# Optimization experiments

Measured on AMD Instinct MI355X. Metric: run time of the kernel, lower is better.

## Reference

```python
import jax, jax.numpy as jnp
import numpy as np

B, T, F = 2048, 96, 32
H = 1024
G_EMB = 16
LSTM_IN = F + 11 + 1 + G_EMB  # 60


def _lstm_cell(x, h, c, W_ih, W_hh, b):
    g = x @ W_ih.T + h @ W_hh.T + b
    i, f, gg, o = jnp.split(g, 4, axis=-1)  # torch gate order: i, f, g, o
    c_new = jax.nn.sigmoid(f) * c + jax.nn.sigmoid(i) * jnp.tanh(gg)
    h_new = jax.nn.sigmoid(o) * jnp.tanh(c_new)
    return h_new, c_new


def setup_inputs() -> dict:
    key = jax.random.key(0)
    ks = jax.random.split(key, 26)
    s = 1.0 / np.sqrt(H)
    inp = {
        "dec_known": jax.random.normal(ks[0], (B, T, F), jnp.float32),
        "target_y": jax.random.normal(ks[1], (B, T, 1), jnp.float32),
        "enc_h": jax.random.normal(ks[2], (2, B, H), jnp.float32),
        "enc_c": jax.random.normal(ks[3], (2, B, H), jnp.float32),
        "last_enc_consumption": jax.random.normal(ks[4], (B, 1), jnp.float32),
        "group_ids": jax.random.randint(ks[5], (B,), 0, 1000),
        "cat_province": jax.random.randint(ks[6], (B,), 0, 13),
        "cat_customer_type": jax.random.randint(ks[7], (B,), 0, 2),
        "cat_price_type": jax.random.randint(ks[8], (B,), 0, 5),
        "cat_consumption_level": jax.random.randint(ks[9], (B,), 0, 3),
        # learned parameters
        "group_emb": jax.random.normal(ks[10], (1000, G_EMB), jnp.float32),
        "emb_province": jax.random.normal(ks[11], (13, 4), jnp.float32),
        "emb_customer_type": jax.random.normal(ks[12], (2, 2), jnp.float32),
        "emb_price_type": jax.random.normal(ks[13], (5, 3), jnp.float32),
        "emb_consumption_level": jax.random.normal(ks[14], (3, 2), jnp.float32),
        "W_ih0": jax.random.normal(ks[15], (4 * H, LSTM_IN), jnp.float32) * s,
        "W_hh0": jax.random.normal(ks[16], (4 * H, H), jnp.float32) * s,
        "b0": jax.random.normal(ks[17], (4 * H,), jnp.float32) * s,
        "W_ih1": jax.random.normal(ks[18], (4 * H, H), jnp.float32) * s,
        "W_hh1": jax.random.normal(ks[19], (4 * H, H), jnp.float32) * s,
        "b1": jax.random.normal(ks[20], (4 * H,), jnp.float32) * s,
        "W_proj": jax.random.normal(ks[21], (1, H), jnp.float32) * s,
        "b_proj": jnp.zeros((1,), jnp.float32),
    }
    return inp


def reference(dec_known, target_y, enc_h, enc_c, last_enc_consumption,
              group_ids, cat_province, cat_customer_type, cat_price_type,
              cat_consumption_level, group_emb, emb_province, emb_customer_type,
              emb_price_type, emb_consumption_level, W_ih0, W_hh0, b0,
              W_ih1, W_hh1, b1, W_proj, b_proj):
    b, t, _ = dec_known.shape
    # static per-sample features (categorical + group embeddings)
    cat_emb = jnp.concatenate([
        emb_province[cat_province], emb_customer_type[cat_customer_type],
        emb_price_type[cat_price_type], emb_consumption_level[cat_consumption_level],
    ], axis=-1)  # [B, 11]
    group_vec = group_emb[group_ids]  # [B, 16]
    static = jnp.concatenate([cat_emb, group_vec], axis=-1)  # [B, 27]
    # teacher_forcing_ratio = 1.0 => prev_y is last_enc_consumption then target_y shifted
    prev_y = jnp.concatenate([last_enc_consumption[:, None, :], target_y[:, :-1, :]], axis=1)  # [B,T,1]
    x = jnp.concatenate([
        prev_y, dec_known,
        jnp.broadcast_to(static[:, None, :], (b, t, static.shape[-1])),
    ], axis=-1)  # [B, T, 60]

    def step(carry, x_t):
        h1, c1, h2, c2 = carry
        h1, c1 = _lstm_cell(x_t, h1, c1, W_ih0, W_hh0, b0)
        h2, c2 = _lstm_cell(h1, h2, c2, W_ih1, W_hh1, b1)
        return (h1, c1, h2, c2), h2

    init = (enc_h[0], enc_c[0], enc_h[1], enc_c[1])
    _, hs = jax.lax.scan(step, init, jnp.swapaxes(x, 0, 1))  # hs: [T, B, H]
    y = jnp.einsum('tbh,oh->bto', hs, W_proj) + b_proj  # [B, T, 1]
    return y
```

## Files before the change

### kernel.cpp

```cpp
#include <hip/hip_runtime.h>
#include <hip/hip_bf16.h>
#include <stdint.h>


#define BB  2048
#define TT  96
#define NG  4096
#define NT0 34
#define NT1 64

typedef __bf16 bf16;
typedef __bf16 bf16x8 __attribute__((ext_vector_type(8)));
typedef float  f32x4  __attribute__((ext_vector_type(4)));

__device__ __forceinline__ float sigm(float x) { return 1.0f / (1.0f + __expf(-x)); }
__device__ __forceinline__ float ftanh(float x) { return 2.0f / (1.0f + __expf(-2.0f * x)) - 1.0f; }

#define SB() __builtin_amdgcn_sched_barrier(0)


__global__ __launch_bounds__(256) void build_wf1(const float* __restrict__ Wih1,
                                                 const float* __restrict__ Whh1,
                                                 bf16* __restrict__ Wf) {
  int idx = blockIdx.x * 256 + threadIdx.x;
  if (idx >= 16 * NT1 * 8192) return;
  int j = idx & 7, lane = (idx >> 3) & 63, gf = (idx >> 9) & 7;
  int wg = (idx >> 12) & 1, kt = (idx >> 13) & 63, panel = idx >> 19;
  int np = panel * 256 + wg * 128 + gf * 16 + (lane & 15);
  int k  = kt * 32 + ((lane >> 4) << 3) + j;
  int n  = (np & 3) * 1024 + (np >> 2);
  float v = (k < 1024) ? Wih1[n * 1024 + k] : Whh1[n * 1024 + (k - 1024)];
  Wf[idx] = (bf16)v;
}

__global__ __launch_bounds__(256) void build_wf0(const float* __restrict__ Wih0,
                                                 const float* __restrict__ Whh0,
                                                 bf16* __restrict__ Wf) {
  int idx = blockIdx.x * 256 + threadIdx.x;
  if (idx >= 16 * NT0 * 8192) return;
  int j = idx & 7, lane = (idx >> 3) & 63, gf = (idx >> 9) & 7;
  int wg = (idx >> 12) & 1;
  int rem = idx >> 13;
  int kt = rem % NT0, panel = rem / NT0;
  int np = panel * 256 + wg * 128 + gf * 16 + (lane & 15);
  int k  = kt * 32 + ((lane >> 4) << 3) + j;
  int n  = (np & 3) * 1024 + (np >> 2);
  float v;
  if (k < 60)      v = Wih0[n * 60 + k];
  else if (k < 64) v = 0.0f;
  else             v = Whh0[n * 1024 + (k - 64)];
  Wf[idx] = (bf16)v;
}

__global__ __launch_bounds__(256) void perm_bias(const float* __restrict__ b0,
                                                 const float* __restrict__ b1,
                                                 float* __restrict__ b0p,
                                                 float* __restrict__ b1p) {
  int idx = blockIdx.x * 256 + threadIdx.x;
  if (idx >= NG) return;
  int n = (idx & 3) * 1024 + (idx >> 2);
  b0p[idx] = b0[n];
  b1p[idx] = b1[n];
}

__global__ __launch_bounds__(256) void build_xf(
    const float* __restrict__ dec, const float* __restrict__ ty, const float* __restrict__ lec,
    const int* __restrict__ gid, const int* __restrict__ cp, const int* __restrict__ cct,
    const int* __restrict__ cpt, const int* __restrict__ ccl,
    const float* __restrict__ gemb, const float* __restrict__ ep, const float* __restrict__ ect,
    const float* __restrict__ ept, const float* __restrict__ ecl,
    bf16* __restrict__ Xf) {
  int idx = blockIdx.x * 256 + threadIdx.x;
  if (idx >= BB * TT) return;
  int b = idx / TT, t = idx % TT;
  float xv[64];
  xv[0] = (t == 0) ? lec[b] : ty[b * TT + t - 1];
  const float* d = dec + (size_t)idx * 32;
  #pragma unroll
  for (int k = 0; k < 32; ++k) xv[1 + k] = d[k];
  const float* e;
  e = ep  + cp[b]  * 4;  for (int j = 0; j < 4;  ++j) xv[33 + j] = e[j];
  e = ect + cct[b] * 2;  for (int j = 0; j < 2;  ++j) xv[37 + j] = e[j];
  e = ept + cpt[b] * 3;  for (int j = 0; j < 3;  ++j) xv[39 + j] = e[j];
  e = ecl + ccl[b] * 2;  for (int j = 0; j < 2;  ++j) xv[42 + j] = e[j];
  e = gemb + gid[b] * 16; for (int j = 0; j < 16; ++j) xv[44 + j] = e[j];
  for (int j = 60; j < 64; ++j) xv[j] = 0.0f;
  bf16* slab = Xf + (size_t)t * BB * 64;
  int bt = b >> 4, bl = b & 15;
  #pragma unroll
  for (int k = 0; k < 64; ++k)
    slab[((size_t)(bt * 8 + (k >> 3)) << 7) + bl * 8 + (k & 7)] = (bf16)xv[k];
}

__global__ __launch_bounds__(256) void init_state(const float* __restrict__ enc_h,
                                                  const float* __restrict__ enc_c,
                                                  bf16* __restrict__ H1b,
                                                  bf16* __restrict__ H2b,
                                                  float* __restrict__ c1t,
                                                  float* __restrict__ c2t) {
  int idx = blockIdx.x * 256 + threadIdx.x;
  if (idx >= BB * 1024) return;
  int b = idx >> 10, h = idx & 1023;
  size_t off = ((size_t)((b >> 4) * 128 + (h >> 3)) << 7) + ((b & 15) << 3) + (h & 7);
  H1b[off] = (bf16)enc_h[idx];
  H2b[off] = (bf16)enc_h[(size_t)BB * 1024 + idx];
  c1t[(size_t)h * BB + b] = enc_c[idx];
  c2t[(size_t)h * BB + b] = enc_c[(size_t)BB * 1024 + idx];
}


template <int MODE>
__device__ __forceinline__ void body(
    int tm, int tn, int t,
    const bf16* __restrict__ P0, const bf16* __restrict__ P1,
    const bf16* __restrict__ Wf, const float* __restrict__ bperm,
    float* __restrict__ ct, bf16* __restrict__ Hout,
    const float* __restrict__ wp, const float* __restrict__ bp,
    float* __restrict__ y, bf16* hst_all)
{
  constexpr int NT = MODE ? NT1 : NT0;

  const int tid = threadIdx.x;
  const int lane = tid & 63, w = tid >> 6;
  const int lrow = lane & 15, u = lane >> 4;
  const int wb = w & 1, wg = w >> 1;

  f32x4 acc[8][4];
  #pragma unroll
  for (int gf = 0; gf < 8; ++gf)
    #pragma unroll
    for (int bf = 0; bf < 4; ++bf) acc[gf][bf] = (f32x4){0.f, 0.f, 0.f, 0.f};

  const int aoff = (u << 7) + (lrow << 3);
  const int BtB = (tm >> 4) + wb * 4;

  auto loadA = [&](bf16x8 (&af)[4], int kt) {
    #pragma unroll
    for (int bf = 0; bf < 4; ++bf) {
      const bf16* p;
      if constexpr (MODE == 0) {
        p = (kt < 2) ? P0 + ((size_t)((BtB + bf) * 8 + kt * 4) << 7) + aoff
                     : P1 + ((size_t)((BtB + bf) * 128 + (kt - 2) * 4) << 7) + aoff;
      } else {
        p = (kt < 32) ? P0 + ((size_t)((BtB + bf) * 128 + kt * 4) << 7) + aoff
                      : P1 + ((size_t)((BtB + bf) * 128 + (kt - 32) * 4) << 7) + aoff;
      }
      af[bf] = *reinterpret_cast<const bf16x8*>(p);
    }
  };

  const bf16* wfbase = Wf + (size_t)(tn >> 8) * NT * 8192 + wg * 4096 + lane * 8;
  auto loadW = [&](bf16x8 (&wf)[8], int kt) {
    const bf16* p = wfbase + (size_t)kt * 8192;
    #pragma unroll
    for (int gf = 0; gf < 8; ++gf)
      wf[gf] = *reinterpret_cast<const bf16x8*>(p + gf * 512);
  };

  bf16x8 afA[4], afB[4], wfA[8], wfB[8];

  loadA(afA, 0); loadW(wfA, 0);
  for (int kt = 0; kt < NT; kt += 2) {
    if (kt + 1 < NT) { loadA(afB, kt + 1); loadW(wfB, kt + 1); }
    SB();
    __builtin_amdgcn_s_setprio(1);
    #pragma unroll
    for (int gf = 0; gf < 8; ++gf)
      #pragma unroll
      for (int bf = 0; bf < 4; ++bf)
        acc[gf][bf] = __builtin_amdgcn_mfma_f32_16x16x32_bf16(wfA[gf], afA[bf], acc[gf][bf], 0, 0, 0);
    __builtin_amdgcn_s_setprio(0);
    if (kt + 2 < NT) { loadA(afA, kt + 2); loadW(wfA, kt + 2); }
    SB();
    __builtin_amdgcn_s_setprio(1);
    #pragma unroll
    for (int gf = 0; gf < 8; ++gf)
      #pragma unroll
      for (int bf = 0; bf < 4; ++bf)
        acc[gf][bf] = __builtin_amdgcn_mfma_f32_16x16x32_bf16(wfB[gf], afB[bf], acc[gf][bf], 0, 0, 0);
    __builtin_amdgcn_s_setprio(0);
  }

  bf16* hst = hst_all + w * 2048;
  const int hq = (tn >> 2) + wg * 32;
  const int bgb = tm + wb * 64;
  float yp[4] = {0.f, 0.f, 0.f, 0.f};

  #pragma unroll
  for (int gf = 0; gf < 8; ++gf) {
    int hg = hq + gf * 4 + u;
    f32x4 bv = *reinterpret_cast<const f32x4*>(&bperm[hg * 4]);
    float wph = 0.f;
    if constexpr (MODE == 1) wph = wp[hg];
    #pragma unroll
    for (int bf = 0; bf < 4; ++bf) {
      int bg = bgb + bf * 16 + lrow;
      float gi = acc[gf][bf][0] + bv[0];
      float gf_ = acc[gf][bf][1] + bv[1];
      float gg = acc[gf][bf][2] + bv[2];
      float go = acc[gf][bf][3] + bv[3];
      float* cp_ = ct + (size_t)hg * BB + bg;
      float c = *cp_;
      float cn = sigm(gf_) * c + sigm(gi) * ftanh(gg);
      float hn = sigm(go) * ftanh(cn);
      *cp_ = cn;
      hst[(bf * 16 + lrow) * 32 + gf * 4 + u] = (bf16)hn;
      if constexpr (MODE == 1) yp[bf] += hn * wph;
    }
  }

  asm volatile("s_waitcnt lgkmcnt(0)" ::: "memory");
  SB();

  #pragma unroll
  for (int q = 0; q < 4; ++q) {
    int chunk = q * 64 + lane;
    int row = chunk >> 2, seg = chunk & 3;
    bf16x8 v = *reinterpret_cast<const bf16x8*>(&hst[row * 32 + seg * 8]);
    size_t off = ((size_t)(((bgb >> 4) + (row >> 4)) * 128 + (hq >> 3) + seg) << 7)
               + ((row & 15) << 3);
    *reinterpret_cast<bf16x8*>(&Hout[off]) = v;
  }

  if constexpr (MODE == 1) {
    #pragma unroll
    for (int bf = 0; bf < 4; ++bf) {
      float s = yp[bf];
      s += __shfl_xor(s, 16);
      s += __shfl_xor(s, 32);
      if (lane < 16)
        atomicAdd(&y[(size_t)(bgb + bf * 16 + lane) * TT + t], s);
    }
  } else {
    if (tn == 0 && tid < 128) y[(size_t)(tm + tid) * TT + t] = bp[0];
  }
}

__global__ __launch_bounds__(256, 2) void step_kernel(
    const bf16* __restrict__ H1in, const bf16* __restrict__ H2in,
    bf16* __restrict__ H1out, bf16* __restrict__ H2out,
    const bf16* __restrict__ Xf,
    const bf16* __restrict__ Wf0, const bf16* __restrict__ Wf1,
    const float* __restrict__ b0p, const float* __restrict__ b1p,
    float* __restrict__ c1t, float* __restrict__ c2t,
    const float* __restrict__ wp, const float* __restrict__ bp,
    float* __restrict__ y, int t2, int only_l1) {
  __shared__ alignas(16) bf16 hst_all[4 * 2048];
  int bid = (int)blockIdx.x;
  if (only_l1 || bid >= 256) {
    int v = only_l1 ? bid : bid - 256;
    int t1 = t2 + 1;
    if (t1 >= TT) return;
    int x = v & 7, r = v >> 3;
    int tm = (r & 15) << 7;
    int tn = ((x << 1) + (r >> 4)) << 8;
    body<0>(tm, tn, t1, Xf + (size_t)t1 * BB * 64, H1in,
            Wf0, b0p, c1t, H1out, nullptr, bp, y, hst_all);
  } else {
    int x = bid & 7, r = bid >> 3;
    int tm = (r & 15) << 7;
    int tn = ((x << 1) + (r >> 4)) << 8;
    body<1>(tm, tn, t2, H1in, H2in,
            Wf1, b1p, c2t, H2out, wp, nullptr, y, hst_all);
  }
}


extern "C" void kernel_launch(void* const* d_in, const int* in_sizes, int n_in,
                              void* d_out, int out_size, void* d_ws, size_t ws_size,
                              hipStream_t stream) {
  const float* dec   = (const float*)d_in[0];
  const float* ty    = (const float*)d_in[1];
  const float* enc_h = (const float*)d_in[2];
  const float* enc_c = (const float*)d_in[3];
  const float* lec   = (const float*)d_in[4];
  const int*   gid   = (const int*)d_in[5];
  const int*   cp    = (const int*)d_in[6];
  const int*   cct   = (const int*)d_in[7];
  const int*   cpt   = (const int*)d_in[8];
  const int*   ccl   = (const int*)d_in[9];
  const float* gemb  = (const float*)d_in[10];
  const float* ep    = (const float*)d_in[11];
  const float* ect   = (const float*)d_in[12];
  const float* ept   = (const float*)d_in[13];
  const float* ecl   = (const float*)d_in[14];
  const float* Wih0  = (const float*)d_in[15];
  const float* Whh0  = (const float*)d_in[16];
  const float* b0    = (const float*)d_in[17];
  const float* Wih1  = (const float*)d_in[18];
  const float* Whh1  = (const float*)d_in[19];
  const float* b1    = (const float*)d_in[20];
  const float* wp    = (const float*)d_in[21];
  const float* bp    = (const float*)d_in[22];
  float* y = (float*)d_out;

  char* ws = (char*)d_ws;
  bf16* Wf1   = (bf16*)ws;  ws += (size_t)16 * NT1 * 8192 * 2;
  bf16* Wf0   = (bf16*)ws;  ws += (size_t)16 * NT0 * 8192 * 2;
  bf16* Xf    = (bf16*)ws;  ws += (size_t)BB * TT * 64 * 2;
  bf16* H1a   = (bf16*)ws;  ws += (size_t)BB * 1024 * 2;
  bf16* H1b   = (bf16*)ws;  ws += (size_t)BB * 1024 * 2;
  bf16* H2a   = (bf16*)ws;  ws += (size_t)BB * 1024 * 2;
  bf16* H2b   = (bf16*)ws;  ws += (size_t)BB * 1024 * 2;
  float* c1t  = (float*)ws; ws += (size_t)BB * 1024 * 4;
  float* c2t  = (float*)ws; ws += (size_t)BB * 1024 * 4;
  float* b0p  = (float*)ws; ws += (size_t)NG * 4;
  float* b1p  = (float*)ws; ws += (size_t)NG * 4;

  build_wf1<<<(16 * NT1 * 8192) / 256, 256, 0, stream>>>(Wih1, Whh1, Wf1);
  build_wf0<<<(16 * NT0 * 8192 + 255) / 256, 256, 0, stream>>>(Wih0, Whh0, Wf0);
  perm_bias<<<NG / 256, 256, 0, stream>>>(b0, b1, b0p, b1p);
  build_xf<<<(BB * TT + 255) / 256, 256, 0, stream>>>(dec, ty, lec, gid, cp, cct, cpt, ccl,
                                                      gemb, ep, ect, ept, ecl, Xf);
  init_state<<<(BB * 1024) / 256, 256, 0, stream>>>(enc_h, enc_c, H1b, H2b, c1t, c2t);

  step_kernel<<<256, 256, 0, stream>>>(H1b, nullptr, H1a, nullptr, Xf, Wf0, Wf1,
                                       b0p, b1p, c1t, c2t, wp, bp, y, -1, 1);
  for (int t = 0; t < TT; ++t) {
    bf16* h1i = (t & 1) ? H1b : H1a;
    bf16* h1o = (t & 1) ? H1a : H1b;
    bf16* h2i = (t & 1) ? H2a : H2b;
    bf16* h2o = (t & 1) ? H2b : H2a;
    step_kernel<<<512, 256, 0, stream>>>(h1i, h2i, h1o, h2o, Xf, Wf0, Wf1,
                                         b0p, b1p, c1t, c2t, wp, bp, y, t, 0);
  }
}
```

Baseline: 5.921 ms.

## Enlarge per-wave tile to 128 batch rows with two waves per block

```diff
diff --git a/kernel.cpp b/kernel.cpp
--- a/kernel.cpp
+++ b/kernel.cpp
@@ -123,20 +123,19 @@
   const int tid = threadIdx.x;
   const int lane = tid & 63, w = tid >> 6;
   const int lrow = lane & 15, u = lane >> 4;
-  const int wb = w & 1, wg = w >> 1;
-
-  f32x4 acc[8][4];
+
+  f32x4 acc[8][8];
   #pragma unroll
   for (int gf = 0; gf < 8; ++gf)
     #pragma unroll
-    for (int bf = 0; bf < 4; ++bf) acc[gf][bf] = (f32x4){0.f, 0.f, 0.f, 0.f};
+    for (int bf = 0; bf < 8; ++bf) acc[gf][bf] = (f32x4){0.f, 0.f, 0.f, 0.f};
 
   const int aoff = (u << 7) + (lrow << 3);
-  const int BtB = (tm >> 4) + wb * 4;
-
-  auto loadA = [&](bf16x8 (&af)[4], int kt) {
-    #pragma unroll
-    for (int bf = 0; bf < 4; ++bf) {
+  const int BtB = tm >> 4;
+
+  auto loadA = [&](bf16x8 (&af)[8], int kt) {
+    #pragma unroll
+    for (int bf = 0; bf < 8; ++bf) {
       const bf16* p;
       if constexpr (MODE == 0) {
         p = (kt < 2) ? P0 + ((size_t)((BtB + bf) * 8 + kt * 4) << 7) + aoff
@@ -149,7 +148,7 @@
     }
   };
 
-  const bf16* wfbase = Wf + (size_t)(tn >> 8) * NT * 8192 + wg * 4096 + lane * 8;
+  const bf16* wfbase = Wf + (size_t)(tn >> 8) * NT * 8192 + w * 4096 + lane * 8;
   auto loadW = [&](bf16x8 (&wf)[8], int kt) {
     const bf16* p = wfbase + (size_t)kt * 8192;
     #pragma unroll
@@ -157,7 +156,7 @@
       wf[gf] = *reinterpret_cast<const bf16x8*>(p + gf * 512);
   };
 
-  bf16x8 afA[4], afB[4], wfA[8], wfB[8];
+  bf16x8 afA[8], afB[8], wfA[8], wfB[8];
 
   loadA(afA, 0); loadW(wfA, 0);
   for (int kt = 0; kt < NT; kt += 2) {
@@ -167,7 +166,7 @@
     #pragma unroll
     for (int gf = 0; gf < 8; ++gf)
       #pragma unroll
-      for (int bf = 0; bf < 4; ++bf)
+      for (int bf = 0; bf < 8; ++bf)
         acc[gf][bf] = __builtin_amdgcn_mfma_f32_16x16x32_bf16(wfA[gf], afA[bf], acc[gf][bf], 0, 0, 0);
     __builtin_amdgcn_s_setprio(0);
     if (kt + 2 < NT) { loadA(afA, kt + 2); loadW(wfA, kt + 2); }
@@ -176,15 +175,21 @@
     #pragma unroll
     for (int gf = 0; gf < 8; ++gf)
       #pragma unroll
-      for (int bf = 0; bf < 4; ++bf)
+      for (int bf = 0; bf < 8; ++bf)
         acc[gf][bf] = __builtin_amdgcn_mfma_f32_16x16x32_bf16(wfB[gf], afB[bf], acc[gf][bf], 0, 0, 0);
     __builtin_amdgcn_s_setprio(0);
   }
 
-  bf16* hst = hst_all + w * 2048;
-  const int hq = (tn >> 2) + wg * 32;
-  const int bgb = tm + wb * 64;
-  float yp[4] = {0.f, 0.f, 0.f, 0.f};
+  bf16* hst = hst_all + w * (128 * 36);
+  const int hq = (tn >> 2) + w * 32;
+  float yp[8] = {0.f, 0.f, 0.f, 0.f, 0.f, 0.f, 0.f, 0.f};
+
+  float cv[8][8];
+  #pragma unroll
+  for (int gf = 0; gf < 8; ++gf)
+    #pragma unroll
+    for (int bf = 0; bf < 8; ++bf)
+      cv[gf][bf] = ct[(size_t)(hq + gf * 4 + u) * BB + tm + bf * 16 + lrow];
 
   #pragma unroll
   for (int gf = 0; gf < 8; ++gf) {
@@ -193,18 +198,17 @@
     float wph = 0.f;
     if constexpr (MODE == 1) wph = wp[hg];
     #pragma unroll
-    for (int bf = 0; bf < 4; ++bf) {
-      int bg = bgb + bf * 16 + lrow;
+    for (int bf = 0; bf < 8; ++bf) {
+      int bg = tm + bf * 16 + lrow;
       float gi = acc[gf][bf][0] + bv[0];
       float gf_ = acc[gf][bf][1] + bv[1];
       float gg = acc[gf][bf][2] + bv[2];
       float go = acc[gf][bf][3] + bv[3];
-      float* cp_ = ct + (size_t)hg * BB + bg;
-      float c = *cp_;
+      float c = cv[gf][bf];
       float cn = sigm(gf_) * c + sigm(gi) * ftanh(gg);
       float hn = sigm(go) * ftanh(cn);
-      *cp_ = cn;
-      hst[(bf * 16 + lrow) * 32 + gf * 4 + u] = (bf16)hn;
+      ct[(size_t)hg * BB + bg] = cn;
+      hst[(bf * 16 + lrow) * 36 + gf * 4 + u] = (bf16)hn;
       if constexpr (MODE == 1) yp[bf] += hn * wph;
     }
   }
@@ -213,30 +217,30 @@
   SB();
 
   #pragma unroll
-  for (int q = 0; q < 4; ++q) {
+  for (int q = 0; q < 8; ++q) {
     int chunk = q * 64 + lane;
     int row = chunk >> 2, seg = chunk & 3;
-    bf16x8 v = *reinterpret_cast<const bf16x8*>(&hst[row * 32 + seg * 8]);
-    size_t off = ((size_t)(((bgb >> 4) + (row >> 4)) * 128 + (hq >> 3) + seg) << 7)
+    bf16x8 v = *reinterpret_cast<const bf16x8*>(&hst[row * 36 + seg * 8]);
+    size_t off = ((size_t)((BtB + (row >> 4)) * 128 + (hq >> 3) + seg) << 7)
                + ((row & 15) << 3);
     *reinterpret_cast<bf16x8*>(&Hout[off]) = v;
   }
 
   if constexpr (MODE == 1) {
     #pragma unroll
-    for (int bf = 0; bf < 4; ++bf) {
+    for (int bf = 0; bf < 8; ++bf) {
       float s = yp[bf];
       s += __shfl_xor(s, 16);
       s += __shfl_xor(s, 32);
       if (lane < 16)
-        atomicAdd(&y[(size_t)(bgb + bf * 16 + lane) * TT + t], s);
+        atomicAdd(&y[(size_t)(tm + bf * 16 + lane) * TT + t], s);
     }
   } else {
     if (tn == 0 && tid < 128) y[(size_t)(tm + tid) * TT + t] = bp[0];
   }
 }
 
-__global__ __launch_bounds__(256, 2) void step_kernel(
+__global__ __launch_bounds__(128, 1) void step_kernel(
     const bf16* __restrict__ H1in, const bf16* __restrict__ H2in,
     bf16* __restrict__ H1out, bf16* __restrict__ H2out,
     const bf16* __restrict__ Xf,
@@ -245,7 +249,7 @@
     float* __restrict__ c1t, float* __restrict__ c2t,
     const float* __restrict__ wp, const float* __restrict__ bp,
     float* __restrict__ y, int t2, int only_l1) {
-  __shared__ alignas(16) bf16 hst_all[4 * 2048];
+  __shared__ alignas(16) bf16 hst_all[2 * 128 * 36];
   int bid = (int)blockIdx.x;
   if (only_l1 || bid >= 256) {
     int v = only_l1 ? bid : bid - 256;
@@ -314,14 +318,14 @@
                                                       gemb, ep, ect, ept, ecl, Xf);
   init_state<<<(BB * 1024) / 256, 256, 0, stream>>>(enc_h, enc_c, H1b, H2b, c1t, c2t);
 
-  step_kernel<<<256, 256, 0, stream>>>(H1b, nullptr, H1a, nullptr, Xf, Wf0, Wf1,
+  step_kernel<<<256, 128, 0, stream>>>(H1b, nullptr, H1a, nullptr, Xf, Wf0, Wf1,
                                        b0p, b1p, c1t, c2t, wp, bp, y, -1, 1);
   for (int t = 0; t < TT; ++t) {
     bf16* h1i = (t & 1) ? H1b : H1a;
     bf16* h1o = (t & 1) ? H1a : H1b;
     bf16* h2i = (t & 1) ? H2a : H2b;
     bf16* h2o = (t & 1) ? H2b : H2a;
-    step_kernel<<<512, 256, 0, stream>>>(h1i, h2i, h1o, h2o, Xf, Wf0, Wf1,
+    step_kernel<<<512, 128, 0, stream>>>(h1i, h2i, h1o, h2o, Xf, Wf0, Wf1,
                                          b0p, b1p, c1t, c2t, wp, bp, y, t, 0);
   }
 }
```

New measurement: 11.98 ms. +102.4%, slower.
